# Kernel optimization log

Measured on AMD Instinct MI355X. Metric: run time of the kernel, lower is better.

## Reference

```python
import jax, jax.numpy as jnp
from jax import lax
import numpy as np

B, NQ, NT = 32, 256, 512
INF = jnp.float32(1e30)  # stand-in for float('inf') mask fill; all targets are valid here
W_TRANS, W_QPOS, W_ROT = 1.0, 1.0, 1.0


def setup_inputs() -> dict:
    key = jax.random.key(0)
    k1, k2, k3, k4 = jax.random.split(key, 4)
    rot = jax.random.normal(k3, (B, NQ, 4), jnp.float32)
    rot = rot / jnp.linalg.norm(rot, axis=-1, keepdims=True)  # unit quaternions
    return {
        "translation_norm": jax.random.normal(k1, (B, NQ, 3), jnp.float32),
        "qpos_norm": jax.random.normal(k2, (B, NQ, 16), jnp.float32),
        "rotation": rot,
        "norm_pose": jax.random.normal(k4, (B, NT, 23), jnp.float32),
    }


def _l1_cost(p, t):
    # p: [B, NQ, D], t: [B, NT, D] -> [B, NQ, NT] pairwise L1
    return jnp.abs(p[:, :, None, :] - t[:, None, :, :]).sum(-1)


def _final_cost(translation_norm, qpos_norm, rotation, norm_pose):
    valid = jnp.abs(norm_pose).sum(-1) > 0  # [B, NT]
    cost = (W_TRANS * _l1_cost(translation_norm, norm_pose[..., :3])
            + W_QPOS * _l1_cost(qpos_norm, norm_pose[..., 3:19])
            + W_ROT * (1.0 - jnp.abs(jnp.einsum('bqd,bnd->bqn', rotation, norm_pose[..., 19:]))))
    return jnp.where(valid[:, None, :], cost, INF)


def _hungarian(cost):
    """Rectangular LSAP via Jonker-Volgenant shortest augmenting path
    (same algorithm as scipy.optimize.linear_sum_assignment).
    cost: [n, m] with n <= m. Returns col4row [n]: matched column per row."""
    n, m = cost.shape

    def solve_row(carry, cur_row):
        u, v, col4row, row4col = carry

        # --- Dijkstra-like search for the shortest augmenting path ---
        def s_cond(st):
            return st[6] < 0  # until a free column (sink) is found

        def s_body(st):
            i, minVal, SR, SC, spc, path, _sink = st
            SR = SR.at[i].set(True)
            r = minVal + cost[i] - u[i] - v          # reduced costs for row i
            upd = (~SC) & (r < spc)
            spc = jnp.where(upd, r, spc)
            path = jnp.where(upd, i, path)
            masked = jnp.where(SC, INF, spc)
            j = jnp.argmin(masked).astype(jnp.int32)
            minVal = masked[j]
            SC = SC.at[j].set(True)
            free = row4col[j] < 0
            sink = jnp.where(free, j, jnp.int32(-1))
            i = jnp.where(free, i, row4col[j])
            return (i, minVal, SR, SC, spc, path, sink)

        st0 = (cur_row, jnp.float32(0.0),
               jnp.zeros((n,), bool), jnp.zeros((m,), bool),
               jnp.full((m,), INF), jnp.full((m,), -1, jnp.int32), jnp.int32(-1))
        _i, minVal, SR, SC, spc, path, sink = lax.while_loop(s_cond, s_body, st0)

        # --- dual variable updates ---
        spc_row = spc[jnp.clip(col4row, 0, m - 1)]  # [n]; invalid rows masked by SR
        du = jnp.where(jnp.arange(n) == cur_row, minVal, minVal - spc_row)
        u = u + jnp.where(SR, du, 0.0)
        v = v - jnp.where(SC, minVal - spc, 0.0)

        # --- augment along the alternating path back to cur_row ---
        def a_cond(st):
            return ~st[3]

        def a_body(st):
            j, c4r, r4c, _done = st
            i = path[j]
            r4c = r4c.at[j].set(i)
            nj = c4r[i]
            c4r = c4r.at[i].set(j)
            return (nj, c4r, r4c, i == cur_row)

        _, col4row, row4col, _ = lax.while_loop(
            a_cond, a_body, (sink, col4row, row4col, False))
        return (u, v, col4row, row4col), None

    carry0 = (jnp.zeros((n,), jnp.float32), jnp.zeros((m,), jnp.float32),
              jnp.full((n,), -1, jnp.int32), jnp.full((m,), -1, jnp.int32))
    (u, v, col4row, row4col), _ = lax.scan(
        solve_row, carry0, jnp.arange(n, dtype=jnp.int32))
    return col4row


def reference(translation_norm, qpos_norm, rotation, norm_pose):
    final_cost = _final_cost(translation_norm, qpos_norm, rotation, norm_pose)
    # batched Hungarian (replaces per-batch scipy linear_sum_assignment loop)
    per_query_gt_inds = jax.vmap(_hungarian)(final_cost)        # [B, NQ]
    query_matched_mask = jnp.ones_like(per_query_gt_inds)        # all matched (NT >= NQ)
    return final_cost, per_query_gt_inds, query_matched_mask
```

## Files before the change

kernel.cpp:

```cpp
#include <hip/hip_runtime.h>

constexpr int kB  = 32;
constexpr int kNQ = 256;
constexpr int kNT = 512;
constexpr float kInf = 1e30f;
constexpr int kQTile = 32;
constexpr int kSlots = 56;
constexpr int kStride = 544;

__global__ __launch_bounds__(512)
void cost_kernel(const float* __restrict__ trans,
                 const float* __restrict__ qpos,
                 const float* __restrict__ rot,
                 const float* __restrict__ pose,
                 float* __restrict__ cost)
{
    __shared__ float sPose[kNT * 23];

    const int b     = blockIdx.x;
    const int qBase = blockIdx.y * kQTile;
    const int tid   = threadIdx.x;

    const float* pb = pose + (size_t)b * kNT * 23;
    for (int idx = tid; idx < kNT * 23; idx += 512) sPose[idx] = pb[idx];
    __syncthreads();

    float T[23];
    #pragma unroll
    for (int d = 0; d < 23; ++d) T[d] = sPose[tid * 23 + d];

    float s = 0.f;
    #pragma unroll
    for (int d = 0; d < 23; ++d) s += fabsf(T[d]);
    const bool valid = (s > 0.f);

    const float* tr = trans + ((size_t)b * kNQ + qBase) * 3;
    const float* qp = qpos  + ((size_t)b * kNQ + qBase) * 16;
    const float* rt = rot   + ((size_t)b * kNQ + qBase) * 4;
    float* cb = cost + ((size_t)b * kNQ + qBase) * kNT + tid;

    for (int q = 0; q < kQTile; ++q) {
        const float Q0 = tr[q * 3 + 0], Q1 = tr[q * 3 + 1], Q2 = tr[q * 3 + 2];
        float a = fabsf(Q0 - T[0]);
        a += fabsf(Q1 - T[1]);
        a += fabsf(Q2 - T[2]);
        float bsum = 0.f;
        #pragma unroll
        for (int d = 0; d < 16; ++d) bsum += fabsf(qp[q * 16 + d] - T[3 + d]);
        const float r0 = rt[q * 4 + 0], r1 = rt[q * 4 + 1];
        const float r2 = rt[q * 4 + 2], r3 = rt[q * 4 + 3];
        float dot = r0 * T[19] + r1 * T[20] + r2 * T[21] + r3 * T[22];
        float c = (a + bsum) + (1.0f - fabsf(dot));
        cb[(size_t)q * kNT] = valid ? c : kInf;
    }
}

__device__ __forceinline__ unsigned wave_min_u32(unsigned x) {
    unsigned t;
    t = (unsigned)__builtin_amdgcn_update_dpp((int)0xFFFFFFFF, (int)x, 0x111, 0xF, 0xF, false); x = t < x ? t : x;
    t = (unsigned)__builtin_amdgcn_update_dpp((int)0xFFFFFFFF, (int)x, 0x112, 0xF, 0xF, false); x = t < x ? t : x;
    t = (unsigned)__builtin_amdgcn_update_dpp((int)0xFFFFFFFF, (int)x, 0x114, 0xF, 0xF, false); x = t < x ? t : x;
    t = (unsigned)__builtin_amdgcn_update_dpp((int)0xFFFFFFFF, (int)x, 0x118, 0xF, 0xF, false); x = t < x ? t : x;
    t = (unsigned)__builtin_amdgcn_update_dpp((int)0xFFFFFFFF, (int)x, 0x142, 0xF, 0xF, false); x = t < x ? t : x;
    t = (unsigned)__builtin_amdgcn_update_dpp((int)0xFFFFFFFF, (int)x, 0x143, 0xF, 0xF, false); x = t < x ? t : x;
    return (unsigned)__builtin_amdgcn_readlane((int)x, 63);
}

__global__ __launch_bounds__(256)
void hungarian_kernel(const float* __restrict__ cost,
                      float* __restrict__ outInds,
                      float* __restrict__ outMask)
{
    __shared__ float rowCache[kSlots * kStride];
    __shared__ float u[kNQ];
    __shared__ int   col4row[kNQ];
    __shared__ int   row4col[kNT];
    __shared__ int   colBest[kNT];
    __shared__ int   pathL[kNT];
    __shared__ int   rowArg[kNQ];

    const int b   = blockIdx.x;
    const int tid = threadIdx.x;
    const float* __restrict__ C = cost + (size_t)b * kNQ * kNT;

    {
        const float4* Crow = (const float4*)(C + (size_t)tid * kNT);
        float bm = kInf; int barg = 0;
        #pragma unroll 4
        for (int j4 = 0; j4 < kNT / 4; ++j4) {
            float4 cc = Crow[j4];
            const int jb = j4 * 4;
            if (cc.x < bm) { bm = cc.x; barg = jb + 0; }
            if (cc.y < bm) { bm = cc.y; barg = jb + 1; }
            if (cc.z < bm) { bm = cc.z; barg = jb + 2; }
            if (cc.w < bm) { bm = cc.w; barg = jb + 3; }
        }
        u[tid]      = bm;
        rowArg[tid] = barg;
        col4row[tid] = -1;
    }
    row4col[tid] = -1;         row4col[tid + 256] = -1;
    colBest[tid] = 0x7fffffff; colBest[tid + 256] = 0x7fffffff;
    __syncthreads();
    atomicMin(&colBest[rowArg[tid]], tid);
    __syncthreads();
    {
        const int j = rowArg[tid];
        if (colBest[j] == tid) { col4row[tid] = j; row4col[j] = tid; }
    }
    __syncthreads();

    if (tid < 64) {
        const int lane = tid;
        const int laneOff = (lane >> 3) * 68 + (lane & 7) * 8;
        typedef float v2f __attribute__((ext_vector_type(2)));

        float vR[8];
        #pragma unroll
        for (int c = 0; c < 8; ++c) vR[c] = 0.f;

        int tagReg = -1;
        int rr     = 0;

        for (int cur = 0; cur < kNQ; ++cur) {
            if (col4row[cur] >= 0) continue;

            float spcR[8]; int pathR[8]; float mskA[8]; float frzV[8]; int frzP[8];
            #pragma unroll
            for (int c = 0; c < 8; ++c) {
                spcR[c] = kInf; pathR[c] = -1; mskA[c] = 0.f;
                frzV[c] = 0.f;  frzP[c] = -1;
            }
            unsigned scMask = 0;

            int   i      = cur;
            float minVal = 0.f;
            int   sink   = -1;

            for (int guard = 0; guard < kNT + 2 && sink < 0; ++guard) {
                const float ui = u[i];
                float4 p0, p1;
                const unsigned long long hm = __ballot(tagReg == i);
                if (hm != 0ull) {
                    const int slot = (int)__ffsll(hm) - 1;
                    const float4* lp = (const float4*)&rowCache[slot * kStride + laneOff];
                    p0 = lp[0]; p1 = lp[1];
                } else {
                    const float4* rp = (const float4*)(C + (size_t)i * kNT + lane * 8);
                    p0 = rp[0]; p1 = rp[1];
                    if (guard != 0) {
                        float4* wp = (float4*)&rowCache[rr * kStride + laneOff];
                        wp[0] = p0; wp[1] = p1;
                        if (lane == rr) tagReg = i;
                        rr = rr + 1; if (rr == kSlots) rr = 0;
                    }
                }

                const v2f cc2[4] = { {p0.x, p0.y}, {p0.z, p0.w},
                                     {p1.x, p1.y}, {p1.z, p1.w} };
                const v2f mv2 = { minVal, minVal };
                const v2f ui2 = { ui, ui };
                float r8[8];
                #pragma unroll
                for (int p = 0; p < 4; ++p) {
                    const v2f vv = { vR[2*p], vR[2*p + 1] };
                    const v2f rp2 = ((mv2 + cc2[p]) - ui2) - vv;
                    r8[2*p] = rp2.x; r8[2*p + 1] = rp2.y;
                }
                #pragma unroll
                for (int c = 0; c < 8; ++c) {
                    const bool lt = r8[c] < spcR[c];
                    spcR[c]  = lt ? r8[c] : spcR[c];
                    pathR[c] = lt ? i : pathR[c];
                }

                float mskv[8];
                #pragma unroll
                for (int p = 0; p < 4; ++p) {
                    const v2f s2 = { spcR[2*p], spcR[2*p + 1] };
                    const v2f a2 = { mskA[2*p], mskA[2*p + 1] };
                    const v2f m2 = s2 + a2;
                    mskv[2*p] = m2.x; mskv[2*p + 1] = m2.y;
                }
                unsigned sp[8];
                #pragma unroll
                for (int c = 0; c < 8; ++c) sp[c] = __float_as_uint(mskv[c]);
                unsigned mA = sp[1] < sp[0] ? sp[1] : sp[0]; int aA = sp[1] < sp[0] ? 1 : 0;
                unsigned mB = sp[3] < sp[2] ? sp[3] : sp[2]; int aB = sp[3] < sp[2] ? 3 : 2;
                unsigned mC = sp[5] < sp[4] ? sp[5] : sp[4]; int aC = sp[5] < sp[4] ? 5 : 4;
                unsigned mD = sp[7] < sp[6] ? sp[7] : sp[6]; int aD = sp[7] < sp[6] ? 7 : 6;
                unsigned mAB = mB < mA ? mB : mA; int aAB = mB < mA ? aB : aA;
                unsigned mCD = mD < mC ? mD : mC; int aCD = mD < mC ? aD : aC;
                unsigned lvu = mCD < mAB ? mCD : mAB; int lc = mCD < mAB ? aCD : aAB;
                const int lix  = lane * 8 + lc;
                const int spec = row4col[lix];

                const unsigned gmu = wave_min_u32(lvu);
                const unsigned long long bal = __ballot(lvu == gmu);
                const int wl    = (int)__ffsll(bal) - 1;
                const int jstar = __builtin_amdgcn_readlane(lix, wl);
                const int own   = __builtin_amdgcn_readlane(spec, wl);
                minVal = __uint_as_float(gmu);

                if (own < 0) sink = jstar;
                else         i    = own;

                if (wl == lane) {
                    const int lcw = jstar & 7;
                    scMask |= 1u << lcw;
                    #pragma unroll
                    for (int c = 0; c < 8; ++c) {
                        if (c == lcw) {
                            mskA[c] = __builtin_inff();
                            frzV[c] = minVal;
                            frzP[c] = pathR[c];
                        }
                    }
                }
            }

            if (lane == 0) u[cur] += minVal;
            #pragma unroll
            for (int c = 0; c < 8; ++c) {
                if ((scMask >> c) & 1u) {
                    const int j = lane * 8 + c;
                    const int r = row4col[j];
                    const float d = minVal - frzV[c];
                    if (r >= 0) u[r] += d;
                    vR[c] -= d;
                    pathL[j] = frzP[c];
                }
            }
            __threadfence_block();

            if (lane == 0 && sink >= 0) {
                int j = sink;
                while (true) {
                    const int pi = pathL[j];
                    row4col[j] = pi;
                    const int nj = col4row[pi];
                    col4row[pi] = j;
                    if (pi == cur) break;
                    j = nj;
                }
            }
            __threadfence_block();
        }
    }
    __syncthreads();

    outInds[(size_t)b * kNQ + tid] = (float)col4row[tid];
    outMask[(size_t)b * kNQ + tid] = 1.0f;
}

extern "C" void kernel_launch(void* const* d_in, const int* in_sizes, int n_in,
                              void* d_out, int out_size, void* d_ws, size_t ws_size,
                              hipStream_t stream) {
    const float* trans = (const float*)d_in[0];
    const float* qpos  = (const float*)d_in[1];
    const float* rot   = (const float*)d_in[2];
    const float* pose  = (const float*)d_in[3];

    float* out  = (float*)d_out;
    float* cost = out;
    float* inds = out + (size_t)kB * kNQ * kNT;
    float* mask = inds + (size_t)kB * kNQ;

    dim3 g1(kB, kNQ / kQTile);
    cost_kernel<<<g1, 512, 0, stream>>>(trans, qpos, rot, pose, cost);
    hungarian_kernel<<<kB, 256, 0, stream>>>(cost, inds, mask);
}
```

Before: 432.4 us.

## Keep Hungarian assignment state in registers and use direct-mapped row cache

Moves the col4row and row4col arrays into per-lane registers, read with readlane, and runs the augmentation walk wave-wide instead of on lane 0 through shared memory, which removes pathL. The row cache becomes direct-mapped (slot = row & 63), replacing a ballot search with one readlane tag check, and its load is issued speculatively. The cost kernel's query tile shrinks to 8 with the loop unrolled, giving it more blocks. The aim is to cut LDS latency and serial scalar work on the Hungarian critical path, at the cost of more cache conflicts and more register pressure.

```diff
diff --git a/kernel.cpp b/kernel.cpp
--- a/kernel.cpp
+++ b/kernel.cpp
@@ -4,8 +4,8 @@
 constexpr int kNQ = 256;
 constexpr int kNT = 512;
 constexpr float kInf = 1e30f;
-constexpr int kQTile = 32;
-constexpr int kSlots = 56;
+constexpr int kQTile = 8;
+constexpr int kSlots = 64;
 constexpr int kStride = 544;
 
 __global__ __launch_bounds__(512)
@@ -39,6 +39,7 @@
     const float* rt = rot   + ((size_t)b * kNQ + qBase) * 4;
     float* cb = cost + ((size_t)b * kNQ + qBase) * kNT + tid;
 
+    #pragma unroll
     for (int q = 0; q < kQTile; ++q) {
         const float Q0 = tr[q * 3 + 0], Q1 = tr[q * 3 + 1], Q2 = tr[q * 3 + 2];
         float a = fabsf(Q0 - T[0]);
@@ -76,7 +77,6 @@
     __shared__ int   col4row[kNQ];
     __shared__ int   row4col[kNT];
     __shared__ int   colBest[kNT];
-    __shared__ int   pathL[kNT];
     __shared__ int   rowArg[kNQ];
 
     const int b   = blockIdx.x;
@@ -119,17 +119,29 @@
         #pragma unroll
         for (int c = 0; c < 8; ++c) vR[c] = 0.f;
 
+        int c4r0 = col4row[lane * 4 + 0], c4r1 = col4row[lane * 4 + 1];
+        int c4r2 = col4row[lane * 4 + 2], c4r3 = col4row[lane * 4 + 3];
+        int r4c0 = row4col[lane * 8 + 0], r4c1 = row4col[lane * 8 + 1];
+        int r4c2 = row4col[lane * 8 + 2], r4c3 = row4col[lane * 8 + 3];
+        int r4c4 = row4col[lane * 8 + 4], r4c5 = row4col[lane * 8 + 5];
+        int r4c6 = row4col[lane * 8 + 6], r4c7 = row4col[lane * 8 + 7];
+
         int tagReg = -1;
-        int rr     = 0;
 
         for (int cur = 0; cur < kNQ; ++cur) {
-            if (col4row[cur] >= 0) continue;
-
-            float spcR[8]; int pathR[8]; float mskA[8]; float frzV[8]; int frzP[8];
+            {
+                const int ce = cur & 3;
+                const int t01 = (ce & 1) ? c4r1 : c4r0;
+                const int t23 = (ce & 1) ? c4r3 : c4r2;
+                const int cv  = (ce & 2) ? t23 : t01;
+                if (__builtin_amdgcn_readlane(cv, cur >> 2) >= 0) continue;
+            }
+
+            float spcR[8]; int pathR[8]; float mskA[8]; float frzV[8]; int frzP[8]; int frzO[8];
             #pragma unroll
             for (int c = 0; c < 8; ++c) {
                 spcR[c] = kInf; pathR[c] = -1; mskA[c] = 0.f;
-                frzV[c] = 0.f;  frzP[c] = -1;
+                frzV[c] = 0.f;  frzP[c] = -1;  frzO[c] = -1;
             }
             unsigned scMask = 0;
 
@@ -138,22 +150,21 @@
             int   sink   = -1;
 
             for (int guard = 0; guard < kNT + 2 && sink < 0; ++guard) {
+                const int slot = i & (kSlots - 1);
+                float* lrow = &rowCache[slot * kStride + laneOff];
+                const float4 l0 = ((const float4*)lrow)[0];
+                const float4 l1 = ((const float4*)lrow)[1];
                 const float ui = u[i];
+                const int tag = __builtin_amdgcn_readlane(tagReg, slot);
+
                 float4 p0, p1;
-                const unsigned long long hm = __ballot(tagReg == i);
-                if (hm != 0ull) {
-                    const int slot = (int)__ffsll(hm) - 1;
-                    const float4* lp = (const float4*)&rowCache[slot * kStride + laneOff];
-                    p0 = lp[0]; p1 = lp[1];
+                if (tag == i) {
+                    p0 = l0; p1 = l1;
                 } else {
-                    const float4* rp = (const float4*)(C + (size_t)i * kNT + lane * 8);
-                    p0 = rp[0]; p1 = rp[1];
-                    if (guard != 0) {
-                        float4* wp = (float4*)&rowCache[rr * kStride + laneOff];
-                        wp[0] = p0; wp[1] = p1;
-                        if (lane == rr) tagReg = i;
-                        rr = rr + 1; if (rr == kSlots) rr = 0;
-                    }
+                    const float4* gp = (const float4*)(C + (size_t)i * kNT + lane * 8);
+                    p0 = gp[0]; p1 = gp[1];
+                    ((float4*)lrow)[0] = p0; ((float4*)lrow)[1] = p1;
+                    if (lane == slot) tagReg = i;
                 }
 
                 const v2f cc2[4] = { {p0.x, p0.y}, {p0.z, p0.w},
@@ -193,7 +204,14 @@
                 unsigned mCD = mD < mC ? mD : mC; int aCD = mD < mC ? aD : aC;
                 unsigned lvu = mCD < mAB ? mCD : mAB; int lc = mCD < mAB ? aCD : aAB;
                 const int lix  = lane * 8 + lc;
-                const int spec = row4col[lix];
+
+                const int s01 = (lc & 1) ? r4c1 : r4c0;
+                const int s23 = (lc & 1) ? r4c3 : r4c2;
+                const int s45 = (lc & 1) ? r4c5 : r4c4;
+                const int s67 = (lc & 1) ? r4c7 : r4c6;
+                const int sAq = (lc & 2) ? s23 : s01;
+                const int sBq = (lc & 2) ? s67 : s45;
+                const int spec = (lc & 4) ? sBq : sAq;
 
                 const unsigned gmu = wave_min_u32(lvu);
                 const unsigned long long bal = __ballot(lvu == gmu);
@@ -214,38 +232,64 @@
                             mskA[c] = __builtin_inff();
                             frzV[c] = minVal;
                             frzP[c] = pathR[c];
+                            frzO[c] = spec;
                         }
                     }
                 }
             }
 
             if (lane == 0) u[cur] += minVal;
-            #pragma unroll
-            for (int c = 0; c < 8; ++c) {
-                if ((scMask >> c) & 1u) {
-                    const int j = lane * 8 + c;
-                    const int r = row4col[j];
-                    const float d = minVal - frzV[c];
-                    if (r >= 0) u[r] += d;
-                    vR[c] -= d;
-                    pathL[j] = frzP[c];
-                }
-            }
+            int   rr8[8]; float uv8[8];
+            #pragma unroll
+            for (int c = 0; c < 8; ++c) rr8[c] = ((scMask >> c) & 1u) ? frzO[c] : -1;
+            #pragma unroll
+            for (int c = 0; c < 8; ++c) uv8[c] = (rr8[c] >= 0) ? u[rr8[c]] : 0.f;
+            #pragma unroll
+            for (int c = 0; c < 8; ++c)
+                if (rr8[c] >= 0) u[rr8[c]] = uv8[c] + (minVal - frzV[c]);
+            #pragma unroll
+            for (int c = 0; c < 8; ++c)
+                if ((scMask >> c) & 1u) vR[c] -= (minVal - frzV[c]);
             __threadfence_block();
 
-            if (lane == 0 && sink >= 0) {
+            if (sink >= 0) {
                 int j = sink;
                 while (true) {
-                    const int pi = pathL[j];
-                    row4col[j] = pi;
-                    const int nj = col4row[pi];
-                    col4row[pi] = j;
+                    const int je = j & 7;
+                    const int q01 = (je & 1) ? frzP[1] : frzP[0];
+                    const int q23 = (je & 1) ? frzP[3] : frzP[2];
+                    const int q45 = (je & 1) ? frzP[5] : frzP[4];
+                    const int q67 = (je & 1) ? frzP[7] : frzP[6];
+                    const int qA  = (je & 2) ? q23 : q01;
+                    const int qB  = (je & 2) ? q67 : q45;
+                    const int qv  = (je & 4) ? qB : qA;
+                    const int pi  = __builtin_amdgcn_readlane(qv, j >> 3);
+
+                    if (lane == (j >> 3)) {
+                        if (je == 0) r4c0 = pi; if (je == 1) r4c1 = pi;
+                        if (je == 2) r4c2 = pi; if (je == 3) r4c3 = pi;
+                        if (je == 4) r4c4 = pi; if (je == 5) r4c5 = pi;
+                        if (je == 6) r4c6 = pi; if (je == 7) r4c7 = pi;
+                    }
+
+                    const int pe  = pi & 3;
+                    const int w01 = (pe & 1) ? c4r1 : c4r0;
+                    const int w23 = (pe & 1) ? c4r3 : c4r2;
+                    const int wv  = (pe & 2) ? w23 : w01;
+                    const int nj  = __builtin_amdgcn_readlane(wv, pi >> 2);
+                    if (lane == (pi >> 2)) {
+                        if (pe == 0) c4r0 = j; if (pe == 1) c4r1 = j;
+                        if (pe == 2) c4r2 = j; if (pe == 3) c4r3 = j;
+                    }
+
                     if (pi == cur) break;
                     j = nj;
                 }
             }
-            __threadfence_block();
         }
+
+        col4row[lane * 4 + 0] = c4r0; col4row[lane * 4 + 1] = c4r1;
+        col4row[lane * 4 + 2] = c4r2; col4row[lane * 4 + 3] = c4r3;
     }
     __syncthreads();
 
```

New measurement: 479.9 us. 11.0% more time.
